# Performance work log

Hardware: AMD Instinct MI355X
Metric: run time of the kernel (lower is better)

Reference implementation:

```python
import jax, jax.numpy as jnp
import numpy as np

EPS_POS = 0.65
EPS_NEG = 0.4
TAU = 0.03
TEMPERATURE = 0.07


def setup_inputs() -> dict:
    key = jax.random.key(0)
    k1, k2 = jax.random.split(key)
    N, H, W, C = 256, 14, 14, 512  # ResNet18 layer4 features (448x448 frame), pooled audio
    frame = jax.random.normal(k1, (N, H, W, C), dtype=jnp.float32)
    audio = jax.random.normal(k2, (N, C), dtype=jnp.float32)
    return {"frame": frame, "audio": audio}


def reference(frame, audio):
    # frame: [N, H, W, C] vision backbone features; audio: [N, C] pooled audio embedding
    N = frame.shape[0]
    f = frame * jax.lax.rsqrt(jnp.sum(frame * frame, axis=3, keepdims=True))  # l2_normalize axis=3
    a = audio * jax.lax.rsqrt(jnp.sum(audio * audio, axis=1, keepdims=True))  # l2_normalize axis=1

    # S_ii: per-sample spatial similarity map [N, 1, H, W]
    S_ii = jnp.einsum('nhwc,nc->nhw', f, a)[:, None, :, :]
    # S_ij: cross-batch similarity [N, K, H, W] (K == N)
    S_ij = jnp.einsum('nhwc,kc->nkhw', f, a)

    m_ip = jax.nn.sigmoid((S_ii - EPS_POS) / TAU)   # positive soft-mask
    neg = 1.0 - jax.nn.sigmoid((S_ii - EPS_NEG) / TAU)  # hard-negative soft-mask

    # Pi: masked mean of positive similarities -> [N, 1]
    Pi = jnp.sum(m_ip * S_ii, axis=(2, 3)) / jnp.sum(m_ip, axis=(2, 3))

    n_all = jax.nn.sigmoid((S_ij - EPS_POS) / TAU)
    mask = 1.0 - 100.0 * jnp.eye(N, dtype=frame.dtype)  # kill diagonal (self) pairs
    Ni_easy = (jnp.sum(n_all * S_ij, axis=(2, 3)) / jnp.sum(n_all, axis=(2, 3))) * mask  # [N, N]
    Ni_hard = jnp.sum(neg * S_ii, axis=(2, 3)) / jnp.sum(neg, axis=(2, 3))  # [N, 1]

    data = jnp.concatenate([Pi, Ni_hard, Ni_easy], axis=1) * TEMPERATURE  # [N, N+2]

    # __calc_loss (faithful to TF broadcasting: Pi_d is [N,1], Ni_d is [N] -> [N,N] broadcast)
    Pi_d = data[:, 0:1]
    Ni_d = jnp.sum(data[:, 1:], axis=1)
    Pi_e = jnp.exp(Pi_d)
    Ni_e = jnp.exp(Ni_d)
    loss = (-1.0 / N) * jnp.sum(jnp.log(Pi_e / (Pi_e + Ni_e)))
    return loss
```

## Files before the change

kernel.cpp:

```cpp
#include <hip/hip_runtime.h>
#include <stdint.h>

#define N_IMG 256
#define HW 196
#define CDIM 512

#define F_EPS_POS 0.65f
#define F_EPS_NEG 0.40f
#define F_INV_TAU (1.0f/0.03f)
#define F_TEMP 0.07f

typedef __attribute__((ext_vector_type(8))) short bf16x8;
typedef __attribute__((ext_vector_type(8))) unsigned short u16x8;
typedef __attribute__((ext_vector_type(4))) float f32x4;

__device__ __forceinline__ unsigned short f2bf(float x){
    unsigned int u = __float_as_uint(x);
    u = (u + 0x7FFFu + ((u >> 16) & 1u)) >> 16;
    return (unsigned short)u;
}
__device__ __forceinline__ float sigm(float x){ return 1.0f/(1.0f + __expf(-x)); }

__global__ void audio_norm_k(const float* __restrict__ audio,
                             unsigned short* __restrict__ abf){
    int k = blockIdx.x, t = threadIdx.x;
    __shared__ float red[256];
    float v0 = audio[k*CDIM + t];
    float v1 = audio[k*CDIM + t + 256];
    red[t] = v0*v0 + v1*v1;
    __syncthreads();
    for (int s = 128; s > 0; s >>= 1){
        if (t < s) red[t] += red[t+s];
        __syncthreads();
    }
    float rrt = 1.0f / sqrtf(red[0]);
    abf[k*CDIM + t]       = f2bf(v0*rrt);
    abf[k*CDIM + t + 256] = f2bf(v1*rrt);
}

__global__ __launch_bounds__(256, 2)
void main_k(const float* __restrict__ frame,
            const unsigned short* __restrict__ abf,
            float* __restrict__ num, float* __restrict__ den,
            float* __restrict__ hnum, float* __restrict__ hden){
    __shared__ unsigned short fT[2][16*520];
    __shared__ float rnormS[2][16];

    const int t    = threadIdx.x;
    const int n    = blockIdx.x >> 1;
    const int k0   = (blockIdx.x & 1) * 128;
    const int lane = t & 63, wid = t >> 6;
    const int col  = lane & 15, quad = lane >> 4;
    const int kg0  = k0 + wid*32 + col;
    const int kg1  = kg0 + 16;

    bf16x8 B0[16], B1[16];
    {
        const unsigned short* b0p = abf + (size_t)kg0*CDIM + quad*8;
        const unsigned short* b1p = abf + (size_t)kg1*CDIM + quad*8;
        #pragma unroll
        for (int j = 0; j < 16; ++j){
            B0[j] = *(const bf16x8*)(b0p + j*32);
            B1[j] = *(const bf16x8*)(b1p + j*32);
        }
    }

    const int r  = t >> 4;
    const int c0 = (t & 15) * 32;

    float en0=0.f, en1=0.f, ed0=0.f, ed1=0.f;
    float hn0=0.f, hn1=0.f, hd0=0.f, hd1=0.f;

    auto loadT = [&](int pt, float4* v){
        int p = pt*16 + r;
        if (p < HW){
            const float4* src = (const float4*)(frame + ((size_t)n*HW + p)*CDIM + c0);
            #pragma unroll
            for (int i = 0; i < 8; ++i) v[i] = src[i];
        } else {
            #pragma unroll
            for (int i = 0; i < 8; ++i) v[i] = make_float4(0.f,0.f,0.f,0.f);
        }
    };
    auto storeT = [&](const float4* v, int buf){
        float ss = 0.f;
        #pragma unroll
        for (int i = 0; i < 8; ++i)
            ss += v[i].x*v[i].x + v[i].y*v[i].y + v[i].z*v[i].z + v[i].w*v[i].w;
        unsigned short* dst = fT[buf] + r*520 + c0;
        #pragma unroll
        for (int j = 0; j < 4; ++j){
            float4 a = v[2*j], b = v[2*j+1];
            u16x8 u = { f2bf(a.x), f2bf(a.y), f2bf(a.z), f2bf(a.w),
                        f2bf(b.x), f2bf(b.y), f2bf(b.z), f2bf(b.w) };
            *(u16x8*)(dst + j*8) = u;
        }
        ss += __shfl_xor(ss, 1, 64);
        ss += __shfl_xor(ss, 2, 64);
        ss += __shfl_xor(ss, 4, 64);
        ss += __shfl_xor(ss, 8, 64);
        if ((t & 15) == 0)
            rnormS[buf][r] = (ss > 0.f) ? (1.0f/sqrtf(ss)) : 0.f;
    };

    {
        float4 v[8];
        loadT(0, v);
        storeT(v, 0);
    }
    __syncthreads();

    for (int pt = 0; pt < 13; ++pt){
        const int cur = pt & 1, nxt = cur ^ 1;
        const bool hasNext = (pt < 12);

        float4 v[8];
        if (hasNext) loadT(pt + 1, v);

        const unsigned short* fbase = fT[cur] + col*520 + quad*8;
        f32x4 acc0 = {0.f,0.f,0.f,0.f};
        f32x4 acc1 = {0.f,0.f,0.f,0.f};
        #pragma unroll
        for (int j = 0; j < 16; ++j){
            bf16x8 a = *(const bf16x8*)(fbase + j*32);
            acc0 = __builtin_amdgcn_mfma_f32_16x16x32_bf16(a, B0[j], acc0, 0, 0, 0);
            acc1 = __builtin_amdgcn_mfma_f32_16x16x32_bf16(a, B1[j], acc1, 0, 0, 0);
        }
        f32x4 rn4 = *(const f32x4*)(&rnormS[cur][quad*4]);
        #pragma unroll
        for (int rr = 0; rr < 4; ++rr){
            int prow = pt*16 + quad*4 + rr;
            if (prow < HW){
                float s0 = acc0[rr] * rn4[rr];
                float s1 = acc1[rr] * rn4[rr];
                float w0 = sigm((s0 - F_EPS_POS) * F_INV_TAU);
                float w1 = sigm((s1 - F_EPS_POS) * F_INV_TAU);
                en0 += w0*s0; ed0 += w0;
                en1 += w1*s1; ed1 += w1;
                if (kg0 == n){ float wn = 1.f - sigm((s0 - F_EPS_NEG) * F_INV_TAU); hn0 += wn*s0; hd0 += wn; }
                if (kg1 == n){ float wn = 1.f - sigm((s1 - F_EPS_NEG) * F_INV_TAU); hn1 += wn*s1; hd1 += wn; }
            }
        }

        if (hasNext) storeT(v, nxt);
        __syncthreads();
    }

    en0 += __shfl_xor(en0, 16, 64); en0 += __shfl_xor(en0, 32, 64);
    ed0 += __shfl_xor(ed0, 16, 64); ed0 += __shfl_xor(ed0, 32, 64);
    en1 += __shfl_xor(en1, 16, 64); en1 += __shfl_xor(en1, 32, 64);
    ed1 += __shfl_xor(ed1, 16, 64); ed1 += __shfl_xor(ed1, 32, 64);
    hn0 += __shfl_xor(hn0, 16, 64); hn0 += __shfl_xor(hn0, 32, 64);
    hd0 += __shfl_xor(hd0, 16, 64); hd0 += __shfl_xor(hd0, 32, 64);
    hn1 += __shfl_xor(hn1, 16, 64); hn1 += __shfl_xor(hn1, 32, 64);
    hd1 += __shfl_xor(hd1, 16, 64); hd1 += __shfl_xor(hd1, 32, 64);

    if (quad == 0){
        num[n*N_IMG + kg0] = en0;  den[n*N_IMG + kg0] = ed0;
        num[n*N_IMG + kg1] = en1;  den[n*N_IMG + kg1] = ed1;
        if (kg0 == n){ hnum[n] = hn0; hden[n] = hd0; }
        if (kg1 == n){ hnum[n] = hn1; hden[n] = hd1; }
    }
}

__global__ void pd_k(const float* __restrict__ num, const float* __restrict__ den,
                     const float* __restrict__ hnum, const float* __restrict__ hden,
                     float* __restrict__ Pi_d, float* __restrict__ Ni_d){
    int nn = blockIdx.x, t = threadIdx.x;
    __shared__ float red[256];
    __shared__ float diagv;
    float ratio = num[nn*N_IMG + t] / den[nn*N_IMG + t];
    if (t == nn) diagv = ratio;
    red[t] = ratio * (t == nn ? -99.f : 1.f);
    __syncthreads();
    for (int s = 128; s > 0; s >>= 1){
        if (t < s) red[t] += red[t+s];
        __syncthreads();
    }
    if (t == 0){
        Pi_d[nn] = F_TEMP * diagv;
        Ni_d[nn] = F_TEMP * (hnum[nn]/hden[nn] + red[0]);
    }
}

__global__ void loss_k(const float* __restrict__ Pi_d, const float* __restrict__ Ni_d,
                       float* __restrict__ out){
    int i = blockIdx.x, j = threadIdx.x;
    __shared__ float red[256];
    float x = Ni_d[j] - Pi_d[i];
    red[j] = (x > 20.f) ? x : log1pf(__expf(x));
    __syncthreads();
    for (int s = 128; s > 0; s >>= 1){
        if (j < s) red[j] += red[j+s];
        __syncthreads();
    }
    if (j == 0) atomicAdd(out, red[0] * (1.0f/(float)N_IMG));
}

extern "C" void kernel_launch(void* const* d_in, const int* in_sizes, int n_in,
                              void* d_out, int out_size, void* d_ws, size_t ws_size,
                              hipStream_t stream) {
    const float* frame = (const float*)d_in[0];
    const float* audio = (const float*)d_in[1];
    float* out = (float*)d_out;
    char* ws = (char*)d_ws;

    unsigned short* abf = (unsigned short*)(ws);
    float* num  = (float*)(ws + 262144);
    float* den  = (float*)(ws + 524288);
    float* hnum = (float*)(ws + 786432);
    float* hden = (float*)(ws + 787456);
    float* Pi_d = (float*)(ws + 788480);
    float* Ni_d = (float*)(ws + 789504);

    hipMemsetAsync(out, 0, sizeof(float), stream);

    audio_norm_k<<<N_IMG, 256, 0, stream>>>(audio, abf);
    main_k<<<N_IMG*2, 256, 0, stream>>>(frame, abf, num, den, hnum, hden);
    pd_k<<<N_IMG, 256, 0, stream>>>(num, den, hnum, hden, Pi_d, Ni_d);
    loss_k<<<N_IMG, 256, 0, stream>>>(Pi_d, Ni_d, out);
}
```

Before: 178.8 us.

## Split main kernel into four K-quarters per image with XCD-aware block swizzle

Each block now handles 64 audio columns instead of 128, so the grid doubles to 1024 blocks and each wave keeps only one B fragment set, halving B registers. Launch bounds rise to 4 blocks per CU for more occupancy. Block indices are swizzled so the four blocks sharing an image land on the same XCD for L2 reuse of frame data. The frame load pattern becomes interleaved and coalesced, and out-of-range rows are clamped instead of zero-filled. The cost is that each frame tile is now read and converted by four blocks instead of two.

```diff
diff --git a/kernel.cpp b/kernel.cpp
--- a/kernel.cpp
+++ b/kernel.cpp
@@ -38,7 +38,7 @@
     abf[k*CDIM + t + 256] = f2bf(v1*rrt);
 }
 
-__global__ __launch_bounds__(256, 2)
+__global__ __launch_bounds__(256, 4)
 void main_k(const float* __restrict__ frame,
             const unsigned short* __restrict__ abf,
             float* __restrict__ num, float* __restrict__ den,
@@ -46,60 +46,52 @@
     __shared__ unsigned short fT[2][16*520];
     __shared__ float rnormS[2][16];
 
-    const int t    = threadIdx.x;
-    const int n    = blockIdx.x >> 1;
-    const int k0   = (blockIdx.x & 1) * 128;
+    const int t = threadIdx.x;
+    const int w  = ((blockIdx.x & 7) << 7) + (blockIdx.x >> 3);
+    const int n  = w >> 2;
+    const int k0 = (w & 3) << 6;
     const int lane = t & 63, wid = t >> 6;
     const int col  = lane & 15, quad = lane >> 4;
-    const int kg0  = k0 + wid*32 + col;
-    const int kg1  = kg0 + 16;
-
-    bf16x8 B0[16], B1[16];
+    const int kg   = k0 + wid*16 + col;
+
+    bf16x8 B[16];
     {
-        const unsigned short* b0p = abf + (size_t)kg0*CDIM + quad*8;
-        const unsigned short* b1p = abf + (size_t)kg1*CDIM + quad*8;
-        #pragma unroll
-        for (int j = 0; j < 16; ++j){
-            B0[j] = *(const bf16x8*)(b0p + j*32);
-            B1[j] = *(const bf16x8*)(b1p + j*32);
-        }
-    }
-
-    const int r  = t >> 4;
-    const int c0 = (t & 15) * 32;
-
-    float en0=0.f, en1=0.f, ed0=0.f, ed1=0.f;
-    float hn0=0.f, hn1=0.f, hd0=0.f, hd1=0.f;
+        const unsigned short* bp = abf + (size_t)kg*CDIM + quad*8;
+        #pragma unroll
+        for (int j = 0; j < 16; ++j) B[j] = *(const bf16x8*)(bp + j*32);
+    }
+
+    const int r = t >> 4;
+    const int c = t & 15;
+
+    float en = 0.f, ed = 0.f, hn = 0.f, hd = 0.f;
 
     auto loadT = [&](int pt, float4* v){
         int p = pt*16 + r;
-        if (p < HW){
-            const float4* src = (const float4*)(frame + ((size_t)n*HW + p)*CDIM + c0);
-            #pragma unroll
-            for (int i = 0; i < 8; ++i) v[i] = src[i];
-        } else {
-            #pragma unroll
-            for (int i = 0; i < 8; ++i) v[i] = make_float4(0.f,0.f,0.f,0.f);
-        }
+        if (p > HW-1) p = HW-1;
+        const float4* src = (const float4*)(frame + ((size_t)n*HW + p)*CDIM);
+        #pragma unroll
+        for (int i = 0; i < 8; ++i)
+            v[i] = src[(c << 1) + (i & 1) + (i >> 1)*32];
     };
     auto storeT = [&](const float4* v, int buf){
         float ss = 0.f;
         #pragma unroll
         for (int i = 0; i < 8; ++i)
             ss += v[i].x*v[i].x + v[i].y*v[i].y + v[i].z*v[i].z + v[i].w*v[i].w;
-        unsigned short* dst = fT[buf] + r*520 + c0;
+        unsigned short* dst = fT[buf] + r*520 + c*8;
         #pragma unroll
         for (int j = 0; j < 4; ++j){
             float4 a = v[2*j], b = v[2*j+1];
             u16x8 u = { f2bf(a.x), f2bf(a.y), f2bf(a.z), f2bf(a.w),
                         f2bf(b.x), f2bf(b.y), f2bf(b.z), f2bf(b.w) };
-            *(u16x8*)(dst + j*8) = u;
+            *(u16x8*)(dst + j*128) = u;
         }
         ss += __shfl_xor(ss, 1, 64);
         ss += __shfl_xor(ss, 2, 64);
         ss += __shfl_xor(ss, 4, 64);
         ss += __shfl_xor(ss, 8, 64);
-        if ((t & 15) == 0)
+        if (c == 0)
             rnormS[buf][r] = (ss > 0.f) ? (1.0f/sqrtf(ss)) : 0.f;
     };
 
@@ -118,27 +110,21 @@
         if (hasNext) loadT(pt + 1, v);
 
         const unsigned short* fbase = fT[cur] + col*520 + quad*8;
-        f32x4 acc0 = {0.f,0.f,0.f,0.f};
-        f32x4 acc1 = {0.f,0.f,0.f,0.f};
+        f32x4 acc = {0.f,0.f,0.f,0.f};
         #pragma unroll
         for (int j = 0; j < 16; ++j){
             bf16x8 a = *(const bf16x8*)(fbase + j*32);
-            acc0 = __builtin_amdgcn_mfma_f32_16x16x32_bf16(a, B0[j], acc0, 0, 0, 0);
-            acc1 = __builtin_amdgcn_mfma_f32_16x16x32_bf16(a, B1[j], acc1, 0, 0, 0);
+            acc = __builtin_amdgcn_mfma_f32_16x16x32_bf16(a, B[j], acc, 0, 0, 0);
         }
         f32x4 rn4 = *(const f32x4*)(&rnormS[cur][quad*4]);
         #pragma unroll
         for (int rr = 0; rr < 4; ++rr){
             int prow = pt*16 + quad*4 + rr;
             if (prow < HW){
-                float s0 = acc0[rr] * rn4[rr];
-                float s1 = acc1[rr] * rn4[rr];
-                float w0 = sigm((s0 - F_EPS_POS) * F_INV_TAU);
-                float w1 = sigm((s1 - F_EPS_POS) * F_INV_TAU);
-                en0 += w0*s0; ed0 += w0;
-                en1 += w1*s1; ed1 += w1;
-                if (kg0 == n){ float wn = 1.f - sigm((s0 - F_EPS_NEG) * F_INV_TAU); hn0 += wn*s0; hd0 += wn; }
-                if (kg1 == n){ float wn = 1.f - sigm((s1 - F_EPS_NEG) * F_INV_TAU); hn1 += wn*s1; hd1 += wn; }
+                float s  = acc[rr] * rn4[rr];
+                float wp = sigm((s - F_EPS_POS) * F_INV_TAU);
+                en += wp*s; ed += wp;
+                if (kg == n){ float wn = 1.f - sigm((s - F_EPS_NEG) * F_INV_TAU); hn += wn*s; hd += wn; }
             }
         }
 
@@ -146,20 +132,14 @@
         __syncthreads();
     }
 
-    en0 += __shfl_xor(en0, 16, 64); en0 += __shfl_xor(en0, 32, 64);
-    ed0 += __shfl_xor(ed0, 16, 64); ed0 += __shfl_xor(ed0, 32, 64);
-    en1 += __shfl_xor(en1, 16, 64); en1 += __shfl_xor(en1, 32, 64);
-    ed1 += __shfl_xor(ed1, 16, 64); ed1 += __shfl_xor(ed1, 32, 64);
-    hn0 += __shfl_xor(hn0, 16, 64); hn0 += __shfl_xor(hn0, 32, 64);
-    hd0 += __shfl_xor(hd0, 16, 64); hd0 += __shfl_xor(hd0, 32, 64);
-    hn1 += __shfl_xor(hn1, 16, 64); hn1 += __shfl_xor(hn1, 32, 64);
-    hd1 += __shfl_xor(hd1, 16, 64); hd1 += __shfl_xor(hd1, 32, 64);
+    en += __shfl_xor(en, 16, 64); en += __shfl_xor(en, 32, 64);
+    ed += __shfl_xor(ed, 16, 64); ed += __shfl_xor(ed, 32, 64);
+    hn += __shfl_xor(hn, 16, 64); hn += __shfl_xor(hn, 32, 64);
+    hd += __shfl_xor(hd, 16, 64); hd += __shfl_xor(hd, 32, 64);
 
     if (quad == 0){
-        num[n*N_IMG + kg0] = en0;  den[n*N_IMG + kg0] = ed0;
-        num[n*N_IMG + kg1] = en1;  den[n*N_IMG + kg1] = ed1;
-        if (kg0 == n){ hnum[n] = hn0; hden[n] = hd0; }
-        if (kg1 == n){ hnum[n] = hn1; hden[n] = hd1; }
+        num[n*N_IMG + kg] = en;  den[n*N_IMG + kg] = ed;
+        if (kg == n){ hnum[n] = hn; hden[n] = hd; }
     }
 }
 
@@ -216,7 +196,7 @@
     hipMemsetAsync(out, 0, sizeof(float), stream);
 
     audio_norm_k<<<N_IMG, 256, 0, stream>>>(audio, abf);
-    main_k<<<N_IMG*2, 256, 0, stream>>>(frame, abf, num, den, hnum, hden);
+    main_k<<<N_IMG*4, 256, 0, stream>>>(frame, abf, num, den, hnum, hden);
     pd_k<<<N_IMG, 256, 0, stream>>>(num, den, hnum, hden, Pi_d, Ni_d);
     loss_k<<<N_IMG, 256, 0, stream>>>(Pi_d, Ni_d, out);
 }
```

Measured after the change: 195.0 us. +9.0%, slower.

## Process all 256 audio columns per block to read frame data once

Applied to the files above, without the earlier changes.

The main kernel now launches one 512-thread block per image instead of two 256-thread blocks that each covered half of the audio columns. Each frame tile is therefore read from global memory once rather than twice. The load pattern also changes so each wavefront reads two full contiguous rows. Out-of-range rows are clamped to the last row instead of being zero-filled, which relies on the existing prow<HW mask in the epilogue. The larger block with many register-resident B fragments may raise register pressure under the new launch bounds.

```diff
diff --git a/kernel.cpp b/kernel.cpp
--- a/kernel.cpp
+++ b/kernel.cpp
@@ -11,7 +11,7 @@
 #define F_TEMP 0.07f
 
 typedef __attribute__((ext_vector_type(8))) short bf16x8;
-typedef __attribute__((ext_vector_type(8))) unsigned short u16x8;
+typedef __attribute__((ext_vector_type(4))) unsigned short u16x4;
 typedef __attribute__((ext_vector_type(4))) float f32x4;
 
 __device__ __forceinline__ unsigned short f2bf(float x){
@@ -38,7 +38,7 @@
     abf[k*CDIM + t + 256] = f2bf(v1*rrt);
 }
 
-__global__ __launch_bounds__(256, 2)
+__global__ __launch_bounds__(512, 2)
 void main_k(const float* __restrict__ frame,
             const unsigned short* __restrict__ abf,
             float* __restrict__ num, float* __restrict__ den,
@@ -47,11 +47,10 @@
     __shared__ float rnormS[2][16];
 
     const int t    = threadIdx.x;
-    const int n    = blockIdx.x >> 1;
-    const int k0   = (blockIdx.x & 1) * 128;
+    const int n    = blockIdx.x;
     const int lane = t & 63, wid = t >> 6;
     const int col  = lane & 15, quad = lane >> 4;
-    const int kg0  = k0 + wid*32 + col;
+    const int kg0  = wid*32 + col;
     const int kg1  = kg0 + 16;
 
     bf16x8 B0[16], B1[16];
@@ -65,46 +64,47 @@
         }
     }
 
-    const int r  = t >> 4;
-    const int c0 = (t & 15) * 32;
+    const int r0 = 2*wid, r1 = r0 + 1;
 
     float en0=0.f, en1=0.f, ed0=0.f, ed1=0.f;
     float hn0=0.f, hn1=0.f, hd0=0.f, hd1=0.f;
 
     auto loadT = [&](int pt, float4* v){
-        int p = pt*16 + r;
-        if (p < HW){
-            const float4* src = (const float4*)(frame + ((size_t)n*HW + p)*CDIM + c0);
-            #pragma unroll
-            for (int i = 0; i < 8; ++i) v[i] = src[i];
-        } else {
-            #pragma unroll
-            for (int i = 0; i < 8; ++i) v[i] = make_float4(0.f,0.f,0.f,0.f);
-        }
+        int p0 = pt*16 + r0; if (p0 > HW-1) p0 = HW-1;
+        int p1 = pt*16 + r1; if (p1 > HW-1) p1 = HW-1;
+        const float4* s0 = (const float4*)(frame + ((size_t)n*HW + p0)*CDIM);
+        const float4* s1 = (const float4*)(frame + ((size_t)n*HW + p1)*CDIM);
+        v[0] = s0[lane]; v[1] = s0[lane + 64];
+        v[2] = s1[lane]; v[3] = s1[lane + 64];
     };
     auto storeT = [&](const float4* v, int buf){
-        float ss = 0.f;
-        #pragma unroll
-        for (int i = 0; i < 8; ++i)
-            ss += v[i].x*v[i].x + v[i].y*v[i].y + v[i].z*v[i].z + v[i].w*v[i].w;
-        unsigned short* dst = fT[buf] + r*520 + c0;
-        #pragma unroll
-        for (int j = 0; j < 4; ++j){
-            float4 a = v[2*j], b = v[2*j+1];
-            u16x8 u = { f2bf(a.x), f2bf(a.y), f2bf(a.z), f2bf(a.w),
-                        f2bf(b.x), f2bf(b.y), f2bf(b.z), f2bf(b.w) };
-            *(u16x8*)(dst + j*8) = u;
-        }
-        ss += __shfl_xor(ss, 1, 64);
-        ss += __shfl_xor(ss, 2, 64);
-        ss += __shfl_xor(ss, 4, 64);
-        ss += __shfl_xor(ss, 8, 64);
-        if ((t & 15) == 0)
-            rnormS[buf][r] = (ss > 0.f) ? (1.0f/sqrtf(ss)) : 0.f;
+        float ss0 = v[0].x*v[0].x + v[0].y*v[0].y + v[0].z*v[0].z + v[0].w*v[0].w
+                  + v[1].x*v[1].x + v[1].y*v[1].y + v[1].z*v[1].z + v[1].w*v[1].w;
+        float ss1 = v[2].x*v[2].x + v[2].y*v[2].y + v[2].z*v[2].z + v[2].w*v[2].w
+                  + v[3].x*v[3].x + v[3].y*v[3].y + v[3].z*v[3].z + v[3].w*v[3].w;
+        unsigned short* d0 = fT[buf] + r0*520;
+        unsigned short* d1 = fT[buf] + r1*520;
+        u16x4 u0 = { f2bf(v[0].x), f2bf(v[0].y), f2bf(v[0].z), f2bf(v[0].w) };
+        u16x4 u1 = { f2bf(v[1].x), f2bf(v[1].y), f2bf(v[1].z), f2bf(v[1].w) };
+        u16x4 u2 = { f2bf(v[2].x), f2bf(v[2].y), f2bf(v[2].z), f2bf(v[2].w) };
+        u16x4 u3 = { f2bf(v[3].x), f2bf(v[3].y), f2bf(v[3].z), f2bf(v[3].w) };
+        *(u16x4*)(d0 + lane*4)       = u0;
+        *(u16x4*)(d0 + 256 + lane*4) = u1;
+        *(u16x4*)(d1 + lane*4)       = u2;
+        *(u16x4*)(d1 + 256 + lane*4) = u3;
+        #pragma unroll
+        for (int d = 1; d < 64; d <<= 1){
+            ss0 += __shfl_xor(ss0, d, 64);
+            ss1 += __shfl_xor(ss1, d, 64);
+        }
+        if (lane == 0){
+            rnormS[buf][r0] = (ss0 > 0.f) ? (1.0f/sqrtf(ss0)) : 0.f;
+            rnormS[buf][r1] = (ss1 > 0.f) ? (1.0f/sqrtf(ss1)) : 0.f;
+        }
     };
 
     {
-        float4 v[8];
+        float4 v[4];
         loadT(0, v);
         storeT(v, 0);
     }
@@ -114,7 +114,7 @@
         const int cur = pt & 1, nxt = cur ^ 1;
         const bool hasNext = (pt < 12);
 
-        float4 v[8];
+        float4 v[4];
         if (hasNext) loadT(pt + 1, v);
 
         const unsigned short* fbase = fT[cur] + col*520 + quad*8;
@@ -216,7 +216,7 @@
     hipMemsetAsync(out, 0, sizeof(float), stream);
 
     audio_norm_k<<<N_IMG, 256, 0, stream>>>(audio, abf);
-    main_k<<<N_IMG*2, 256, 0, stream>>>(frame, abf, num, den, hnum, hden);
+    main_k<<<N_IMG, 512, 0, stream>>>(frame, abf, num, den, hnum, hden);
     pd_k<<<N_IMG, 256, 0, stream>>>(num, den, hnum, hden, Pi_d, Ni_d);
     loss_k<<<N_IMG, 256, 0, stream>>>(Pi_d, Ni_d, out);
 }
```

Result: no change. 175.9 us (-1.6%).

## Split blocks over spatial halves with all 256 audio columns per block

Applied to the files above, without the earlier changes.

Each block now covers half of the spatial positions (112 rows) against all 256 audio vectors, using 512 threads, instead of all positions against 128 audio vectors. The frame tile is streamed along the channel dimension in 64-channel stages into a padded LDS buffer, with 7 accumulator tiles per wave held in registers. Each image's frame data is now read by only one block rather than two, halving global frame traffic. The cost is partial sums that pd_k must combine, much higher register pressure from the 14 accumulators plus the pinned B fragments, and row norms that are applied only after all stages finish.

```diff
diff --git a/kernel.cpp b/kernel.cpp
--- a/kernel.cpp
+++ b/kernel.cpp
@@ -38,20 +38,22 @@
     abf[k*CDIM + t + 256] = f2bf(v1*rrt);
 }
 
-__global__ __launch_bounds__(256, 2)
+__global__ __launch_bounds__(512) __attribute__((amdgpu_waves_per_eu(2, 2)))
 void main_k(const float* __restrict__ frame,
             const unsigned short* __restrict__ abf,
-            float* __restrict__ num, float* __restrict__ den,
-            float* __restrict__ hnum, float* __restrict__ hden){
-    __shared__ unsigned short fT[2][16*520];
-    __shared__ float rnormS[2][16];
+            float* __restrict__ np0, float* __restrict__ dp0,
+            float* __restrict__ np1, float* __restrict__ dp1,
+            float* __restrict__ hn_p0, float* __restrict__ hd_p0,
+            float* __restrict__ hn_p1, float* __restrict__ hd_p1){
+    __shared__ unsigned short A[2][112*72];
+    __shared__ float rnS[112];
 
     const int t    = threadIdx.x;
     const int n    = blockIdx.x >> 1;
-    const int k0   = (blockIdx.x & 1) * 128;
+    const int half = blockIdx.x & 1;
     const int lane = t & 63, wid = t >> 6;
     const int col  = lane & 15, quad = lane >> 4;
-    const int kg0  = k0 + wid*32 + col;
+    const int kg0  = wid*32 + col;
     const int kg1  = kg0 + 16;
 
     bf16x8 B0[16], B1[16];
@@ -64,75 +66,90 @@
             B1[j] = *(const bf16x8*)(b1p + j*32);
         }
     }
-
-    const int r  = t >> 4;
-    const int c0 = (t & 15) * 32;
+#define ANCH8(a,b,c,d,e,f,g,h) \
+    asm volatile("" : "+v"(a),"+v"(b),"+v"(c),"+v"(d),"+v"(e),"+v"(f),"+v"(g),"+v"(h))
+    ANCH8(B0[0],B0[1],B0[2],B0[3],B0[4],B0[5],B0[6],B0[7]);
+    ANCH8(B0[8],B0[9],B0[10],B0[11],B0[12],B0[13],B0[14],B0[15]);
+    ANCH8(B1[0],B1[1],B1[2],B1[3],B1[4],B1[5],B1[6],B1[7]);
+    ANCH8(B1[8],B1[9],B1[10],B1[11],B1[12],B1[13],B1[14],B1[15]);
+#undef ANCH8
+
+    const int  srow = t >> 2;
+    const int  sc   = (t & 3) * 16;
+    const bool sact = (srow < 112);
+    int prow = half*112 + srow; if (prow > HW-1) prow = HW-1;
+    const float* gsrc = frame + ((size_t)n*HW + prow)*CDIM + sc;
+
+    float ss = 0.f;
+    float4 v[4];
+
+    auto sload = [&](int s){
+        if (sact){
+            const float4* p = (const float4*)(gsrc + s*64);
+            v[0] = p[0]; v[1] = p[1]; v[2] = p[2]; v[3] = p[3];
+        }
+    };
+    auto sstore = [&](int buf){
+        if (sact){
+            ss += v[0].x*v[0].x + v[0].y*v[0].y + v[0].z*v[0].z + v[0].w*v[0].w
+                + v[1].x*v[1].x + v[1].y*v[1].y + v[1].z*v[1].z + v[1].w*v[1].w
+                + v[2].x*v[2].x + v[2].y*v[2].y + v[2].z*v[2].z + v[2].w*v[2].w
+                + v[3].x*v[3].x + v[3].y*v[3].y + v[3].z*v[3].z + v[3].w*v[3].w;
+            u16x8 w0 = { f2bf(v[0].x), f2bf(v[0].y), f2bf(v[0].z), f2bf(v[0].w),
+                         f2bf(v[1].x), f2bf(v[1].y), f2bf(v[1].z), f2bf(v[1].w) };
+            u16x8 w1 = { f2bf(v[2].x), f2bf(v[2].y), f2bf(v[2].z), f2bf(v[2].w),
+                         f2bf(v[3].x), f2bf(v[3].y), f2bf(v[3].z), f2bf(v[3].w) };
+            unsigned short* d = &A[buf][srow*72 + sc];
+            *(u16x8*)(d)     = w0;
+            *(u16x8*)(d + 8) = w1;
+        }
+    };
+
+    f32x4 acc0[7], acc1[7];
+    #pragma unroll
+    for (int m = 0; m < 7; ++m){
+        acc0[m] = (f32x4){0.f,0.f,0.f,0.f};
+        acc1[m] = (f32x4){0.f,0.f,0.f,0.f};
+    }
+
+    sload(0); sstore(0);
+    __syncthreads();
+
+    #pragma unroll
+    for (int s = 0; s < 8; ++s){
+        if (s < 7) sload(s + 1);
+        const int buf = s & 1;
+        #pragma unroll
+        for (int m = 0; m < 7; ++m){
+            #pragma unroll
+            for (int ks = 0; ks < 2; ++ks){
+                bf16x8 a = *(const bf16x8*)&A[buf][(m*16 + col)*72 + ks*32 + quad*8];
+                acc0[m] = __builtin_amdgcn_mfma_f32_16x16x32_bf16(a, B0[2*s+ks], acc0[m], 0, 0, 0);
+                acc1[m] = __builtin_amdgcn_mfma_f32_16x16x32_bf16(a, B1[2*s+ks], acc1[m], 0, 0, 0);
+            }
+        }
+        if (s < 7) sstore((s + 1) & 1);
+        __syncthreads();
+    }
+
+    ss += __shfl_xor(ss, 1, 64);
+    ss += __shfl_xor(ss, 2, 64);
+    if (sact && (t & 3) == 0)
+        rnS[srow] = (ss > 0.f) ? (1.0f/sqrtf(ss)) : 0.f;
+    __syncthreads();
 
     float en0=0.f, en1=0.f, ed0=0.f, ed1=0.f;
     float hn0=0.f, hn1=0.f, hd0=0.f, hd1=0.f;
-
-    auto loadT = [&](int pt, float4* v){
-        int p = pt*16 + r;
-        if (p < HW){
-            const float4* src = (const float4*)(frame + ((size_t)n*HW + p)*CDIM + c0);
-            #pragma unroll
-            for (int i = 0; i < 8; ++i) v[i] = src[i];
-        } else {
-            #pragma unroll
-            for (int i = 0; i < 8; ++i) v[i] = make_float4(0.f,0.f,0.f,0.f);
-        }
-    };
-    auto storeT = [&](const float4* v, int buf){
-        float ss = 0.f;
-        #pragma unroll
-        for (int i = 0; i < 8; ++i)
-            ss += v[i].x*v[i].x + v[i].y*v[i].y + v[i].z*v[i].z + v[i].w*v[i].w;
-        unsigned short* dst = fT[buf] + r*520 + c0;
-        #pragma unroll
-        for (int j = 0; j < 4; ++j){
-            float4 a = v[2*j], b = v[2*j+1];
-            u16x8 u = { f2bf(a.x), f2bf(a.y), f2bf(a.z), f2bf(a.w),
-                        f2bf(b.x), f2bf(b.y), f2bf(b.z), f2bf(b.w) };
-            *(u16x8*)(dst + j*8) = u;
-        }
-        ss += __shfl_xor(ss, 1, 64);
-        ss += __shfl_xor(ss, 2, 64);
-        ss += __shfl_xor(ss, 4, 64);
-        ss += __shfl_xor(ss, 8, 64);
-        if ((t & 15) == 0)
-            rnormS[buf][r] = (ss > 0.f) ? (1.0f/sqrtf(ss)) : 0.f;
-    };
-
-    {
-        float4 v[8];
-        loadT(0, v);
-        storeT(v, 0);
-    }
-    __syncthreads();
-
-    for (int pt = 0; pt < 13; ++pt){
-        const int cur = pt & 1, nxt = cur ^ 1;
-        const bool hasNext = (pt < 12);
-
-        float4 v[8];
-        if (hasNext) loadT(pt + 1, v);
-
-        const unsigned short* fbase = fT[cur] + col*520 + quad*8;
-        f32x4 acc0 = {0.f,0.f,0.f,0.f};
-        f32x4 acc1 = {0.f,0.f,0.f,0.f};
-        #pragma unroll
-        for (int j = 0; j < 16; ++j){
-            bf16x8 a = *(const bf16x8*)(fbase + j*32);
-            acc0 = __builtin_amdgcn_mfma_f32_16x16x32_bf16(a, B0[j], acc0, 0, 0, 0);
-            acc1 = __builtin_amdgcn_mfma_f32_16x16x32_bf16(a, B1[j], acc1, 0, 0, 0);
-        }
-        f32x4 rn4 = *(const f32x4*)(&rnormS[cur][quad*4]);
+    #pragma unroll
+    for (int m = 0; m < 7; ++m){
         #pragma unroll
         for (int rr = 0; rr < 4; ++rr){
-            int prow = pt*16 + quad*4 + rr;
-            if (prow < HW){
-                float s0 = acc0[rr] * rn4[rr];
-                float s1 = acc1[rr] * rn4[rr];
+            int row = m*16 + quad*4 + rr;
+            int pr  = half*112 + row;
+            if (pr < HW){
+                float rn = rnS[row];
+                float s0 = acc0[m][rr] * rn;
+                float s1 = acc1[m][rr] * rn;
                 float w0 = sigm((s0 - F_EPS_POS) * F_INV_TAU);
                 float w1 = sigm((s1 - F_EPS_POS) * F_INV_TAU);
                 en0 += w0*s0; ed0 += w0;
@@ -141,9 +158,6 @@
                 if (kg1 == n){ float wn = 1.f - sigm((s1 - F_EPS_NEG) * F_INV_TAU); hn1 += wn*s1; hd1 += wn; }
             }
         }
-
-        if (hasNext) storeT(v, nxt);
-        __syncthreads();
     }
 
     en0 += __shfl_xor(en0, 16, 64); en0 += __shfl_xor(en0, 32, 64);
@@ -155,21 +169,26 @@
     hn1 += __shfl_xor(hn1, 16, 64); hn1 += __shfl_xor(hn1, 32, 64);
     hd1 += __shfl_xor(hd1, 16, 64); hd1 += __shfl_xor(hd1, 32, 64);
 
+    float* npH = half ? np1 : np0;
+    float* dpH = half ? dp1 : dp0;
     if (quad == 0){
-        num[n*N_IMG + kg0] = en0;  den[n*N_IMG + kg0] = ed0;
-        num[n*N_IMG + kg1] = en1;  den[n*N_IMG + kg1] = ed1;
-        if (kg0 == n){ hnum[n] = hn0; hden[n] = hd0; }
-        if (kg1 == n){ hnum[n] = hn1; hden[n] = hd1; }
-    }
-}
-
-__global__ void pd_k(const float* __restrict__ num, const float* __restrict__ den,
-                     const float* __restrict__ hnum, const float* __restrict__ hden,
+        npH[n*N_IMG + kg0] = en0;  dpH[n*N_IMG + kg0] = ed0;
+        npH[n*N_IMG + kg1] = en1;  dpH[n*N_IMG + kg1] = ed1;
+        if (kg0 == n){ (half?hn_p1:hn_p0)[n] = hn0; (half?hd_p1:hd_p0)[n] = hd0; }
+        if (kg1 == n){ (half?hn_p1:hn_p0)[n] = hn1; (half?hd_p1:hd_p0)[n] = hd1; }
+    }
+}
+
+__global__ void pd_k(const float* __restrict__ np0, const float* __restrict__ dp0,
+                     const float* __restrict__ np1, const float* __restrict__ dp1,
+                     const float* __restrict__ hn_p0, const float* __restrict__ hd_p0,
+                     const float* __restrict__ hn_p1, const float* __restrict__ hd_p1,
                      float* __restrict__ Pi_d, float* __restrict__ Ni_d){
     int nn = blockIdx.x, t = threadIdx.x;
     __shared__ float red[256];
     __shared__ float diagv;
-    float ratio = num[nn*N_IMG + t] / den[nn*N_IMG + t];
+    float ratio = (np0[nn*N_IMG + t] + np1[nn*N_IMG + t])
+                / (dp0[nn*N_IMG + t] + dp1[nn*N_IMG + t]);
     if (t == nn) diagv = ratio;
     red[t] = ratio * (t == nn ? -99.f : 1.f);
     __syncthreads();
@@ -179,7 +198,7 @@
     }
     if (t == 0){
         Pi_d[nn] = F_TEMP * diagv;
-        Ni_d[nn] = F_TEMP * (hnum[nn]/hden[nn] + red[0]);
+        Ni_d[nn] = F_TEMP * ((hn_p0[nn]+hn_p1[nn])/(hd_p0[nn]+hd_p1[nn]) + red[0]);
     }
 }
 
@@ -205,18 +224,25 @@
     float* out = (float*)d_out;
     char* ws = (char*)d_ws;
 
-    unsigned short* abf = (unsigned short*)(ws);
-    float* num  = (float*)(ws + 262144);
-    float* den  = (float*)(ws + 524288);
-    float* hnum = (float*)(ws + 786432);
-    float* hden = (float*)(ws + 787456);
-    float* Pi_d = (float*)(ws + 788480);
-    float* Ni_d = (float*)(ws + 789504);
+    unsigned short* abf  = (unsigned short*)(ws);
+    float* np0  = (float*)(ws + 262144);
+    float* dp0  = (float*)(ws + 524288);
+    float* np1  = (float*)(ws + 786432);
+    float* dp1  = (float*)(ws + 1048576);
+    float* hn0  = (float*)(ws + 1310720);
+    float* hd0  = (float*)(ws + 1311744);
+    float* hn1  = (float*)(ws + 1312768);
+    float* hd1  = (float*)(ws + 1313792);
+    float* Pi_d = (float*)(ws + 1314816);
+    float* Ni_d = (float*)(ws + 1315840);
 
     hipMemsetAsync(out, 0, sizeof(float), stream);
 
     audio_norm_k<<<N_IMG, 256, 0, stream>>>(audio, abf);
-    main_k<<<N_IMG*2, 256, 0, stream>>>(frame, abf, num, den, hnum, hden);
-    pd_k<<<N_IMG, 256, 0, stream>>>(num, den, hnum, hden, Pi_d, Ni_d);
+    main_k<<<N_IMG*2, 512, 0, stream>>>(frame, abf,
+                                        np0, dp0, np1, dp1,
+                                        hn0, hd0, hn1, hd1);
+    pd_k<<<N_IMG, 256, 0, stream>>>(np0, dp0, np1, dp1,
+                                    hn0, hd0, hn1, hd1, Pi_d, Ni_d);
     loss_k<<<N_IMG, 256, 0, stream>>>(Pi_d, Ni_d, out);
 }
```

Result: slower. 186.1 us (+4.1%).
